# Kernel tuning notes

Hardware: AMD Instinct MI355X
Metric: run time of the kernel (lower is better)

The kernel has to match this reference:

```python
import jax, jax.numpy as jnp
import numpy as np

B, S, D, H = 2, 2048, 1024, 16
DK = D // H  # 64


def setup_inputs() -> dict:
    key = jax.random.key(0)
    ks = jax.random.split(key, 7)
    q = jax.random.normal(ks[0], (B, S, D), dtype=jnp.float32)
    k = jax.random.normal(ks[1], (B, S, D), dtype=jnp.float32)
    v = jax.random.normal(ks[2], (B, S, D), dtype=jnp.float32)
    # causal 0/1 mask, broadcast over batch and heads
    mask = jnp.tril(jnp.ones((S, S), dtype=jnp.int32))[None, None, :, :]
    scale = 0.02
    Wq = jax.random.normal(ks[3], (D, D), dtype=jnp.float32) * scale
    Wk = jax.random.normal(ks[4], (D, D), dtype=jnp.float32) * scale
    Wv = jax.random.normal(ks[5], (D, D), dtype=jnp.float32) * scale
    Wo = jax.random.normal(ks[6], (D, D), dtype=jnp.float32) * scale
    return {"q": q, "k": k, "v": v, "mask": mask,
            "Wq": Wq, "Wk": Wk, "Wv": Wv, "Wo": Wo}


def _split_heads(x):
    # [B, S, D] -> [B, H, S, DK]
    return x.reshape(B, -1, H, DK).transpose(0, 2, 1, 3)


def reference(q, k, v, mask, Wq, Wk, Wv, Wo):
    # torch nn.Linear(bias=False): y = x @ W.T
    qh = _split_heads(q @ Wq.T)
    kh = _split_heads(k @ Wk.T)
    vh = _split_heads(v @ Wv.T)
    scores = jnp.einsum('bhqd,bhkd->bhqk', qh, kh) / jnp.sqrt(
        jnp.asarray(DK, dtype=jnp.float32))
    scores = jnp.where(mask == 0, -jnp.inf, scores)
    attn = jax.nn.softmax(scores, axis=-1)              # [B, H, S, S]
    out = jnp.einsum('bhqk,bhkd->bhqd', attn, vh)        # [B, H, S, DK]
    concat = out.transpose(0, 2, 1, 3).reshape(B, -1, D)  # [B, S, D]
    return concat @ Wo.T, attn
```

## Files before the change

kernel.cpp:

```cpp
#include <hip/hip_runtime.h>
#include <hip/hip_bf16.h>
#include <stdint.h>

#define B_   2
#define S_   2048
#define D_   1024
#define H_   16
#define DK_  64

typedef __attribute__((ext_vector_type(4))) float          f32x4;
typedef __attribute__((ext_vector_type(8))) __bf16         bf16x8;
typedef __attribute__((ext_vector_type(8))) short          short8;
typedef __attribute__((ext_vector_type(4))) unsigned short u16x4;

__device__ __forceinline__ unsigned short f2bf(float x) {
  union { float f; unsigned u; } un; un.f = x;
  unsigned r = un.u + 0x7fffu + ((un.u >> 16) & 1u);
  return (unsigned short)(r >> 16);
}

__device__ __forceinline__ float fexp2(float x) {
  float r;
  asm("v_exp_f32 %0, %1" : "=v"(r) : "v"(x));
  return r;
}

#define WAIT_LGKM0() asm volatile("s_waitcnt lgkmcnt(0)" ::: "memory")
#define WAIT_VM0()   asm volatile("s_waitcnt vmcnt(0)" ::: "memory")
#define BAR()        __builtin_amdgcn_s_barrier()

#define ASYNC16(gp, lp)                                                         \
  __builtin_amdgcn_global_load_lds(                                             \
      (const __attribute__((address_space(1))) unsigned int*)(const void*)(gp), \
      (__attribute__((address_space(3))) unsigned int*)(void*)(lp), 16, 0, 0)

struct Cvt3 { const float* in[3]; unsigned short* out[3]; };
struct Cvt4 { const float* in[4]; unsigned short* out[4]; };

__global__ __launch_bounds__(256) void cvt3_kernel(Cvt3 a, int n4) {
  int z = blockIdx.y;
  int i = blockIdx.x * 256 + threadIdx.x;
  if (i >= n4) return;
  f32x4 v = *(const f32x4*)(a.in[z] + (size_t)i * 4);
  u16x4 o;
  o.x = f2bf(v.x); o.y = f2bf(v.y); o.z = f2bf(v.z); o.w = f2bf(v.w);
  *(u16x4*)(a.out[z] + (size_t)i * 4) = o;
}

__global__ __launch_bounds__(256) void cvt4_kernel(Cvt4 a, int n4) {
  int z = blockIdx.y;
  int i = blockIdx.x * 256 + threadIdx.x;
  if (i >= n4) return;
  f32x4 v = *(const f32x4*)(a.in[z] + (size_t)i * 4);
  u16x4 o;
  o.x = f2bf(v.x); o.y = f2bf(v.y); o.z = f2bf(v.z); o.w = f2bf(v.w);
  *(u16x4*)(a.out[z] + (size_t)i * 4) = o;
}

template <int BN>
__device__ __forceinline__ void gemm_core(const unsigned short* __restrict__ A,
                                          const unsigned short* __restrict__ W,
                                          unsigned short* sA, unsigned short* sB,
                                          int mBase, int nBase, f32x4 acc[4][BN / 32]) {
  constexpr int NW = BN / 32;
  const int tid = threadIdx.x, wid = tid >> 6, lane = tid & 63;
  const int g16 = lane >> 4, l16 = lane & 15;
  const int wr = wid >> 1, wc = wid & 1;

  auto stage = [&](int buf, int k0) {
#pragma unroll
    for (int i = 0; i < 2; ++i) {
      int L = i * 256 + tid;
      int row = L >> 2;
      int gsw = (L & 3) ^ (row & 3);
      ASYNC16(A + (size_t)(mBase + row) * 1024 + k0 + gsw * 8,
              sA + buf * (128 * 32) + (size_t)(i * 256 + wid * 64) * 8);
    }
#pragma unroll
    for (int i = 0; i < BN / 64; ++i) {
      int L = i * 256 + tid;
      int row = L >> 2;
      int gsw = (L & 3) ^ (row & 3);
      ASYNC16(W + (size_t)(nBase + row) * 1024 + k0 + gsw * 8,
              sB + buf * (BN * 32) + (size_t)(i * 256 + wid * 64) * 8);
    }
  };

  stage(0, 0);
  WAIT_VM0();
  BAR();
  for (int t = 0; t < 32; ++t) {
    const int cur = t & 1;
    if (t < 31) stage(cur ^ 1, (t + 1) * 32);
    const unsigned short* pA = sA + cur * (128 * 32);
    const unsigned short* pB = sB + cur * (BN * 32);
    bf16x8 a[4], b[NW];
#pragma unroll
    for (int mi = 0; mi < 4; ++mi) {
      int rr = wr * 64 + mi * 16 + l16;
      a[mi] = *(const bf16x8*)&pA[rr * 32 + ((g16 ^ (rr & 3)) * 8)];
    }
#pragma unroll
    for (int ni = 0; ni < NW; ++ni) {
      int rr = wc * (BN / 2) + ni * 16 + l16;
      b[ni] = *(const bf16x8*)&pB[rr * 32 + ((g16 ^ (rr & 3)) * 8)];
    }
#pragma unroll
    for (int mi = 0; mi < 4; ++mi)
#pragma unroll
      for (int ni = 0; ni < NW; ++ni)
        acc[mi][ni] = __builtin_amdgcn_mfma_f32_16x16x32_bf16(a[mi], b[ni],
                                                              acc[mi][ni], 0, 0, 0);
    WAIT_LGKM0();
    WAIT_VM0();
    BAR();
  }
}

struct QKVArgs {
  const unsigned short* A[3];
  const unsigned short* W[3];
  unsigned short* O[3];
};

__global__ __launch_bounds__(256) void gemm_qkv(QKVArgs args) {
  __shared__ unsigned short sA[2 * 128 * 32];
  __shared__ unsigned short sB[2 * 128 * 32];
  const int z = blockIdx.z;
  const int mBase = blockIdx.x * 128, nBase = blockIdx.y * 128;
  f32x4 acc[4][4];
  const f32x4 zz = {0.f, 0.f, 0.f, 0.f};
#pragma unroll
  for (int mi = 0; mi < 4; ++mi)
#pragma unroll
    for (int ni = 0; ni < 4; ++ni) acc[mi][ni] = zz;
  gemm_core<128>(args.A[z], args.W[z], sA, sB, mBase, nBase, acc);

  unsigned short* __restrict__ O = args.O[z];
  const int tid = threadIdx.x, wid = tid >> 6, lane = tid & 63;
  const int g16 = lane >> 4, l16 = lane & 15;
  const int wr = wid >> 1, wc = wid & 1;
  const float qscale = 0.125f * 1.44269504088896f;
  const float sc = (z == 0) ? qscale : 1.f;
#pragma unroll
  for (int mi = 0; mi < 4; ++mi)
#pragma unroll
    for (int ni = 0; ni < 4; ++ni)
#pragma unroll
      for (int r = 0; r < 4; ++r) {
        int row = mBase + wr * 64 + mi * 16 + g16 * 4 + r;
        int col = nBase + wc * 64 + ni * 16 + l16;
        int bb = row >> 11, ss = row & 2047;
        int hh = col >> 6,  dd = col & 63;
        unsigned short val = f2bf(acc[mi][ni][r] * sc);
        if (z == 2)
          O[((size_t)(bb * H_ + hh) * DK_ + dd) * S_ + ss] = val;
        else
          O[(((size_t)(bb * H_ + hh)) * S_ + ss) * DK_ + dd] = val;
      }
}

__global__ __launch_bounds__(256) void gemm_out(const unsigned short* __restrict__ A,
                                                const unsigned short* __restrict__ W,
                                                float* __restrict__ Cout) {
  __shared__ unsigned short sA[2 * 128 * 32];
  __shared__ unsigned short sB[2 * 64 * 32];
  const int mBase = blockIdx.x * 128, nBase = blockIdx.y * 64;
  f32x4 acc[4][2];
  const f32x4 zz = {0.f, 0.f, 0.f, 0.f};
#pragma unroll
  for (int mi = 0; mi < 4; ++mi)
#pragma unroll
    for (int ni = 0; ni < 2; ++ni) acc[mi][ni] = zz;
  gemm_core<64>(A, W, sA, sB, mBase, nBase, acc);

  const int tid = threadIdx.x, wid = tid >> 6, lane = tid & 63;
  const int g16 = lane >> 4, l16 = lane & 15;
  const int wr = wid >> 1, wc = wid & 1;
#pragma unroll
  for (int mi = 0; mi < 4; ++mi)
#pragma unroll
    for (int ni = 0; ni < 2; ++ni)
#pragma unroll
      for (int r = 0; r < 4; ++r) {
        int row = mBase + wr * 64 + mi * 16 + g16 * 4 + r;
        int col = nBase + wc * 32 + ni * 16 + l16;
        Cout[(size_t)row * 1024 + col] = acc[mi][ni][r];
      }
}

__global__ __launch_bounds__(256) void attn_kernel(
    const unsigned short* __restrict__ Qh, const unsigned short* __restrict__ Kh,
    const unsigned short* __restrict__ VhT, float* __restrict__ attn,
    unsigned short* __restrict__ Oc) {
  __shared__ unsigned short sK[2 * 64 * 64];
  __shared__ unsigned short sV[2 * 64 * 64];
  __shared__ unsigned short sP[64 * 64];
  const int tid = threadIdx.x, wid = tid >> 6, lane = tid & 63;
  const int g16 = lane >> 4, l16 = lane & 15;
  const int qb = (int)gridDim.x - 1 - (int)blockIdx.x;
  const int bh = blockIdx.y;
  const int qBase = qb * 64;
  const size_t headOff = (size_t)bh * S_ * DK_;
  const int jmax = qb;

  bf16x8 qf[2];
  {
    const unsigned short* qp = Qh + headOff + (size_t)(qBase + wid * 16 + l16) * DK_;
    qf[0] = *(const bf16x8*)(qp + g16 * 8);
    qf[1] = *(const bf16x8*)(qp + 32 + g16 * 8);
  }
  const int rowbase = qBase + wid * 16 + g16 * 4;

  auto stageK = [&](int buf, int j) {
#pragma unroll
    for (int i = 0; i < 2; ++i) {
      int L = i * 256 + tid;
      int krow = L >> 3;
      int gsw = (L & 7) ^ (krow & 7);
      ASYNC16(Kh + headOff + (size_t)(j * 64 + krow) * DK_ + gsw * 8,
              sK + buf * 4096 + (size_t)(i * 256 + wid * 64) * 8);
    }
  };
  auto stageV = [&](int buf, int j) {
#pragma unroll
    for (int i = 0; i < 2; ++i) {
      int L = i * 256 + tid;
      int vrow = L >> 3;
      int gsw = (L & 7) ^ (vrow & 7);
      ASYNC16(VhT + ((size_t)bh * DK_ + vrow) * S_ + j * 64 + gsw * 8,
              sV + buf * 4096 + (size_t)(i * 256 + wid * 64) * 8);
    }
  };

  float l4[4] = {0.f, 0.f, 0.f, 0.f};

  stageK(0, 0);
  WAIT_VM0();
  BAR();
  for (int j = 0; j <= jmax; ++j) {
    const int cur = j & 1;
    if (j < jmax) stageK(cur ^ 1, j + 1);
    const unsigned short* pK = sK + cur * 4096;
    f32x4 sc[4];
    const f32x4 zz = {0.f, 0.f, 0.f, 0.f};
#pragma unroll
    for (int ni = 0; ni < 4; ++ni) sc[ni] = zz;
#pragma unroll
    for (int ks = 0; ks < 2; ++ks)
#pragma unroll
      for (int ni = 0; ni < 4; ++ni) {
        int rr = ni * 16 + l16;
        bf16x8 kb = *(const bf16x8*)&pK[rr * 64 + (((ks * 4 + g16) ^ (rr & 7)) * 8)];
        sc[ni] = __builtin_amdgcn_mfma_f32_16x16x32_bf16(qf[ks], kb, sc[ni], 0, 0, 0);
      }
    if (j < jmax) {
#pragma unroll
      for (int ni = 0; ni < 4; ++ni)
#pragma unroll
        for (int r = 0; r < 4; ++r) l4[r] += fexp2(sc[ni][r]);
    } else {
#pragma unroll
      for (int ni = 0; ni < 4; ++ni) {
        int col = j * 64 + ni * 16 + l16;
#pragma unroll
        for (int r = 0; r < 4; ++r) {
          float e = fexp2(sc[ni][r]);
          l4[r] += (col <= rowbase + r) ? e : 0.f;
        }
      }
    }
    WAIT_LGKM0();
    WAIT_VM0();
    BAR();
  }

  float invl[4];
#pragma unroll
  for (int r = 0; r < 4; ++r) {
    float s = l4[r];
    s += __shfl_xor(s, 1);
    s += __shfl_xor(s, 2);
    s += __shfl_xor(s, 4);
    s += __shfl_xor(s, 8);
    invl[r] = 1.f / s;
  }

  f32x4 oacc[4];
  {
    const f32x4 zz = {0.f, 0.f, 0.f, 0.f};
#pragma unroll
    for (int ni = 0; ni < 4; ++ni) oacc[ni] = zz;
  }

  stageK(0, 0);
  stageV(0, 0);
  WAIT_VM0();
  BAR();
  for (int j = 0; j <= jmax; ++j) {
    const int cur = j & 1;
    if (j < jmax) { stageK(cur ^ 1, j + 1); stageV(cur ^ 1, j + 1); }
    const unsigned short* pK = sK + cur * 4096;
    const unsigned short* pV = sV + cur * 4096;
    f32x4 sc[4];
    const f32x4 zz = {0.f, 0.f, 0.f, 0.f};
#pragma unroll
    for (int ni = 0; ni < 4; ++ni) sc[ni] = zz;
#pragma unroll
    for (int ks = 0; ks < 2; ++ks)
#pragma unroll
      for (int ni = 0; ni < 4; ++ni) {
        int rr = ni * 16 + l16;
        bf16x8 kb = *(const bf16x8*)&pK[rr * 64 + (((ks * 4 + g16) ^ (rr & 7)) * 8)];
        sc[ni] = __builtin_amdgcn_mfma_f32_16x16x32_bf16(qf[ks], kb, sc[ni], 0, 0, 0);
      }
    float* arow = attn + ((size_t)bh * S_ + rowbase) * (size_t)S_ + j * 64;
    if (j < jmax) {
#pragma unroll
      for (int ni = 0; ni < 4; ++ni) {
        int cl = ni * 16 + l16;
#pragma unroll
        for (int r = 0; r < 4; ++r) {
          float p = fexp2(sc[ni][r]) * invl[r];
          arow[(size_t)r * S_ + cl] = p;
          int prow = wid * 16 + g16 * 4 + r;
          sP[prow * 64 + (((cl >> 3) ^ (prow & 7)) * 8) + (cl & 7)] = f2bf(p);
        }
      }
    } else {
#pragma unroll
      for (int ni = 0; ni < 4; ++ni) {
        int cl = ni * 16 + l16;
        int col = j * 64 + cl;
#pragma unroll
        for (int r = 0; r < 4; ++r) {
          float e = fexp2(sc[ni][r]) * invl[r];
          float p = (col <= rowbase + r) ? e : 0.f;
          arow[(size_t)r * S_ + cl] = p;
          int prow = wid * 16 + g16 * 4 + r;
          sP[prow * 64 + (((cl >> 3) ^ (prow & 7)) * 8) + (cl & 7)] = f2bf(p);
        }
      }
    }
#pragma unroll
    for (int ks = 0; ks < 2; ++ks) {
      int pr = wid * 16 + l16;
      bf16x8 pa = *(const bf16x8*)&sP[pr * 64 + (((ks * 4 + g16) ^ (pr & 7)) * 8)];
#pragma unroll
      for (int ni = 0; ni < 4; ++ni) {
        int vr = ni * 16 + l16;
        bf16x8 vb = *(const bf16x8*)&pV[vr * 64 + (((ks * 4 + g16) ^ (vr & 7)) * 8)];
        oacc[ni] = __builtin_amdgcn_mfma_f32_16x16x32_bf16(pa, vb, oacc[ni], 0, 0, 0);
      }
    }
    WAIT_LGKM0();
    WAIT_VM0();
    BAR();
  }

  const int bb = bh >> 4, hh = bh & 15;
#pragma unroll
  for (int ni = 0; ni < 4; ++ni)
#pragma unroll
    for (int r = 0; r < 4; ++r) {
      int srow = rowbase + r;
      Oc[((size_t)bb * S_ + srow) * D_ + hh * 64 + ni * 16 + l16] = f2bf(oacc[ni][r]);
    }

  const int zstart = (jmax + 1) * 64;
  if (zstart < S_) {
    const f32x4 z4 = {0.f, 0.f, 0.f, 0.f};
    int r = tid >> 2;
    int c0 = zstart + (tid & 3) * 4;
    float* rowp = attn + ((size_t)bh * S_ + qBase + r) * (size_t)S_;
    for (int c = c0; c < S_; c += 16)
      *(f32x4*)(rowp + c) = z4;
  }
}

extern "C" void kernel_launch(void* const* d_in, const int* in_sizes, int n_in,
                              void* d_out, int out_size, void* d_ws, size_t ws_size,
                              hipStream_t stream) {
  const float* q  = (const float*)d_in[0];
  const float* k  = (const float*)d_in[1];
  const float* v  = (const float*)d_in[2];
  const float* Wq = (const float*)d_in[4];
  const float* Wk = (const float*)d_in[5];
  const float* Wv = (const float*)d_in[6];
  const float* Wo = (const float*)d_in[7];

  float* out  = (float*)d_out;
  float* attn = out + (size_t)B_ * S_ * D_;

  unsigned short* ws = (unsigned short*)d_ws;
  const size_t BSD = (size_t)B_ * S_ * D_;
  const size_t DD  = (size_t)D_ * D_;
  unsigned short* qb  = ws;
  unsigned short* kb  = qb + BSD;
  unsigned short* vb  = kb + BSD;
  unsigned short* wqb = vb + BSD;
  unsigned short* wkb = wqb + DD;
  unsigned short* wvb = wkb + DD;
  unsigned short* wob = wvb + DD;
  unsigned short* Qh  = wob + DD;
  unsigned short* Kh  = Qh + BSD;
  unsigned short* VhT = Kh + BSD;
  unsigned short* Oc  = VhT + BSD;

  const int n4 = (int)(BSD / 4);
  const int w4 = (int)(DD / 4);
  Cvt3 c3; c3.in[0] = q; c3.in[1] = k; c3.in[2] = v;
  c3.out[0] = qb; c3.out[1] = kb; c3.out[2] = vb;
  cvt3_kernel<<<dim3(n4 / 256, 3), 256, 0, stream>>>(c3, n4);
  Cvt4 c4; c4.in[0] = Wq; c4.in[1] = Wk; c4.in[2] = Wv; c4.in[3] = Wo;
  c4.out[0] = wqb; c4.out[1] = wkb; c4.out[2] = wvb; c4.out[3] = wob;
  cvt4_kernel<<<dim3(w4 / 256, 4), 256, 0, stream>>>(c4, w4);

  QKVArgs args;
  args.A[0] = qb;  args.A[1] = kb;  args.A[2] = vb;
  args.W[0] = wqb; args.W[1] = wkb; args.W[2] = wvb;
  args.O[0] = Qh;  args.O[1] = Kh;  args.O[2] = VhT;
  gemm_qkv<<<dim3(32, 8, 3), 256, 0, stream>>>(args);

  attn_kernel<<<dim3(32, 32), 256, 0, stream>>>(Qh, Kh, VhT, attn, Oc);

  gemm_out<<<dim3(32, 16), 256, 0, stream>>>(Oc, wob, out);
}
```

Before: 282.7 us.

## Merge conversion kernels and swizzle GEMM block order across XCDs

Folds the two fp32-to-bf16 conversion launches into one seven-slice kernel. The projection GEMMs now use a flat grid whose block index is remapped so that consecutive blocks on each XCD (round-robin by 8) share A/W tiles, aiming for better L2 reuse. The manual waitcnt and barrier sequence is replaced with __syncthreads. The merged conversion launches many idle blocks for the smaller weight slices, and the remap assumes an 8-way XCD dispatch.

```diff
diff --git a/kernel.cpp b/kernel.cpp
--- a/kernel.cpp
+++ b/kernel.cpp
@@ -34,22 +34,12 @@
       (const __attribute__((address_space(1))) unsigned int*)(const void*)(gp), \
       (__attribute__((address_space(3))) unsigned int*)(void*)(lp), 16, 0, 0)
 
-struct Cvt3 { const float* in[3]; unsigned short* out[3]; };
-struct Cvt4 { const float* in[4]; unsigned short* out[4]; };
-
-__global__ __launch_bounds__(256) void cvt3_kernel(Cvt3 a, int n4) {
-  int z = blockIdx.y;
-  int i = blockIdx.x * 256 + threadIdx.x;
-  if (i >= n4) return;
-  f32x4 v = *(const f32x4*)(a.in[z] + (size_t)i * 4);
-  u16x4 o;
-  o.x = f2bf(v.x); o.y = f2bf(v.y); o.z = f2bf(v.z); o.w = f2bf(v.w);
-  *(u16x4*)(a.out[z] + (size_t)i * 4) = o;
-}
-
-__global__ __launch_bounds__(256) void cvt4_kernel(Cvt4 a, int n4) {
-  int z = blockIdx.y;
-  int i = blockIdx.x * 256 + threadIdx.x;
+struct CvtAll { const float* in[7]; unsigned short* out[7]; };
+
+__global__ __launch_bounds__(256) void cvt_all(CvtAll a, int n4big, int n4w) {
+  const int z = blockIdx.y;
+  const int n4 = (z < 3) ? n4big : n4w;
+  const int i = blockIdx.x * 256 + threadIdx.x;
   if (i >= n4) return;
   f32x4 v = *(const f32x4*)(a.in[z] + (size_t)i * 4);
   u16x4 o;
@@ -87,8 +77,7 @@
   };
 
   stage(0, 0);
-  WAIT_VM0();
-  BAR();
+  __syncthreads();
   for (int t = 0; t < 32; ++t) {
     const int cur = t & 1;
     if (t < 31) stage(cur ^ 1, (t + 1) * 32);
@@ -111,9 +100,7 @@
       for (int ni = 0; ni < NW; ++ni)
         acc[mi][ni] = __builtin_amdgcn_mfma_f32_16x16x32_bf16(a[mi], b[ni],
                                                               acc[mi][ni], 0, 0, 0);
-    WAIT_LGKM0();
-    WAIT_VM0();
-    BAR();
+    __syncthreads();
   }
 }
 
@@ -126,8 +113,12 @@
 __global__ __launch_bounds__(256) void gemm_qkv(QKVArgs args) {
   __shared__ unsigned short sA[2 * 128 * 32];
   __shared__ unsigned short sB[2 * 128 * 32];
-  const int z = blockIdx.z;
-  const int mBase = blockIdx.x * 128, nBase = blockIdx.y * 128;
+  const int flat = blockIdx.x;
+  const int swz = (flat & 7) * 96 + (flat >> 3);
+  const int z = swz >> 8;
+  const int rem = swz & 255;
+  const int mBase = (rem >> 3) * 128, nBase = (rem & 7) * 128;
+
   f32x4 acc[4][4];
   const f32x4 zz = {0.f, 0.f, 0.f, 0.f};
 #pragma unroll
@@ -165,7 +156,10 @@
                                                 float* __restrict__ Cout) {
   __shared__ unsigned short sA[2 * 128 * 32];
   __shared__ unsigned short sB[2 * 64 * 32];
-  const int mBase = blockIdx.x * 128, nBase = blockIdx.y * 64;
+  const int flat = blockIdx.x;
+  const int swz = (flat & 7) * 64 + (flat >> 3);
+  const int mBase = (swz >> 4) * 128, nBase = (swz & 15) * 64;
+
   f32x4 acc[4][2];
   const f32x4 zz = {0.f, 0.f, 0.f, 0.f};
 #pragma unroll
@@ -409,20 +403,20 @@
 
   const int n4 = (int)(BSD / 4);
   const int w4 = (int)(DD / 4);
-  Cvt3 c3; c3.in[0] = q; c3.in[1] = k; c3.in[2] = v;
-  c3.out[0] = qb; c3.out[1] = kb; c3.out[2] = vb;
-  cvt3_kernel<<<dim3(n4 / 256, 3), 256, 0, stream>>>(c3, n4);
-  Cvt4 c4; c4.in[0] = Wq; c4.in[1] = Wk; c4.in[2] = Wv; c4.in[3] = Wo;
-  c4.out[0] = wqb; c4.out[1] = wkb; c4.out[2] = wvb; c4.out[3] = wob;
-  cvt4_kernel<<<dim3(w4 / 256, 4), 256, 0, stream>>>(c4, w4);
+  CvtAll ca;
+  ca.in[0] = q;  ca.in[1] = k;  ca.in[2] = v;
+  ca.in[3] = Wq; ca.in[4] = Wk; ca.in[5] = Wv; ca.in[6] = Wo;
+  ca.out[0] = qb;  ca.out[1] = kb;  ca.out[2] = vb;
+  ca.out[3] = wqb; ca.out[4] = wkb; ca.out[5] = wvb; ca.out[6] = wob;
+  cvt_all<<<dim3(n4 / 256, 7), 256, 0, stream>>>(ca, n4, w4);
 
   QKVArgs args;
   args.A[0] = qb;  args.A[1] = kb;  args.A[2] = vb;
   args.W[0] = wqb; args.W[1] = wkb; args.W[2] = wvb;
   args.O[0] = Qh;  args.O[1] = Kh;  args.O[2] = VhT;
-  gemm_qkv<<<dim3(32, 8, 3), 256, 0, stream>>>(args);
+  gemm_qkv<<<dim3(768), 256, 0, stream>>>(args);
 
   attn_kernel<<<dim3(32, 32), 256, 0, stream>>>(Qh, Kh, VhT, attn, Oc);
 
-  gemm_out<<<dim3(32, 16), 256, 0, stream>>>(Oc, wob, out);
-}
+  gemm_out<<<dim3(512), 256, 0, stream>>>(Oc, wob, out);
+}
```

Measured after the change: 292.5 us. 3.4% more time.

## Process two 64-row query groups per attention block to reuse K/V tiles

Applied to the files above, without the earlier changes.

Each attention workgroup now handles 128 query rows as two 64-row groups that share every staged K and V tile, which halves the grid from 32x32 to 16x32 blocks. This cuts repeated global-to-LDS traffic for K/V and the per-block launch overhead. The cost is more registers for the doubled Q fragments and accumulators, fewer blocks to spread over the CUs, and some imbalance from the diagonal tile that only the second group computes. Zero-fill of the masked region is adjusted for the larger block.

```diff
diff --git a/kernel.cpp b/kernel.cpp
--- a/kernel.cpp
+++ b/kernel.cpp
@@ -200,17 +200,21 @@
   const int g16 = lane >> 4, l16 = lane & 15;
   const int qb = (int)gridDim.x - 1 - (int)blockIdx.x;
   const int bh = blockIdx.y;
-  const int qBase = qb * 64;
+  const int QBASE = qb * 128;
   const size_t headOff = (size_t)bh * S_ * DK_;
-  const int jmax = qb;
-
-  bf16x8 qf[2];
-  {
-    const unsigned short* qp = Qh + headOff + (size_t)(qBase + wid * 16 + l16) * DK_;
-    qf[0] = *(const bf16x8*)(qp + g16 * 8);
-    qf[1] = *(const bf16x8*)(qp + 32 + g16 * 8);
-  }
-  const int rowbase = qBase + wid * 16 + g16 * 4;
+  const int jmax = 2 * qb + 1;
+
+  bf16x8 qf[2][2];
+#pragma unroll
+  for (int g = 0; g < 2; ++g) {
+    const unsigned short* qp =
+        Qh + headOff + (size_t)(QBASE + g * 64 + wid * 16 + l16) * DK_;
+    qf[g][0] = *(const bf16x8*)(qp + g16 * 8);
+    qf[g][1] = *(const bf16x8*)(qp + 32 + g16 * 8);
+  }
+  int rowbase[2];
+  rowbase[0] = QBASE + wid * 16 + g16 * 4;
+  rowbase[1] = rowbase[0] + 64;
 
   auto stageK = [&](int buf, int j) {
 #pragma unroll
@@ -233,7 +237,7 @@
     }
   };
 
-  float l4[4] = {0.f, 0.f, 0.f, 0.f};
+  float l4[2][4] = {{0.f, 0.f, 0.f, 0.f}, {0.f, 0.f, 0.f, 0.f}};
 
   stageK(0, 0);
   WAIT_VM0();
@@ -242,31 +246,36 @@
     const int cur = j & 1;
     if (j < jmax) stageK(cur ^ 1, j + 1);
     const unsigned short* pK = sK + cur * 4096;
-    f32x4 sc[4];
-    const f32x4 zz = {0.f, 0.f, 0.f, 0.f};
-#pragma unroll
-    for (int ni = 0; ni < 4; ++ni) sc[ni] = zz;
-#pragma unroll
-    for (int ks = 0; ks < 2; ++ks)
-#pragma unroll
-      for (int ni = 0; ni < 4; ++ni) {
-        int rr = ni * 16 + l16;
-        bf16x8 kb = *(const bf16x8*)&pK[rr * 64 + (((ks * 4 + g16) ^ (rr & 7)) * 8)];
-        sc[ni] = __builtin_amdgcn_mfma_f32_16x16x32_bf16(qf[ks], kb, sc[ni], 0, 0, 0);
-      }
-    if (j < jmax) {
-#pragma unroll
-      for (int ni = 0; ni < 4; ++ni)
-#pragma unroll
-        for (int r = 0; r < 4; ++r) l4[r] += fexp2(sc[ni][r]);
-    } else {
-#pragma unroll
-      for (int ni = 0; ni < 4; ++ni) {
-        int col = j * 64 + ni * 16 + l16;
-#pragma unroll
-        for (int r = 0; r < 4; ++r) {
-          float e = fexp2(sc[ni][r]);
-          l4[r] += (col <= rowbase + r) ? e : 0.f;
+#pragma unroll
+    for (int g = 0; g < 2; ++g) {
+      const int dg = 2 * qb + g;
+      if (j > dg) continue;
+      f32x4 sc[4];
+      const f32x4 zz = {0.f, 0.f, 0.f, 0.f};
+#pragma unroll
+      for (int ni = 0; ni < 4; ++ni) sc[ni] = zz;
+#pragma unroll
+      for (int ks = 0; ks < 2; ++ks)
+#pragma unroll
+        for (int ni = 0; ni < 4; ++ni) {
+          int rr = ni * 16 + l16;
+          bf16x8 kb = *(const bf16x8*)&pK[rr * 64 + (((ks * 4 + g16) ^ (rr & 7)) * 8)];
+          sc[ni] = __builtin_amdgcn_mfma_f32_16x16x32_bf16(qf[g][ks], kb, sc[ni], 0, 0, 0);
+        }
+      if (j < dg) {
+#pragma unroll
+        for (int ni = 0; ni < 4; ++ni)
+#pragma unroll
+          for (int r = 0; r < 4; ++r) l4[g][r] += fexp2(sc[ni][r]);
+      } else {
+#pragma unroll
+        for (int ni = 0; ni < 4; ++ni) {
+          int col = j * 64 + ni * 16 + l16;
+#pragma unroll
+          for (int r = 0; r < 4; ++r) {
+            float e = fexp2(sc[ni][r]);
+            l4[g][r] += (col <= rowbase[g] + r) ? e : 0.f;
+          }
         }
       }
     }
@@ -275,22 +284,26 @@
     BAR();
   }
 
-  float invl[4];
-#pragma unroll
-  for (int r = 0; r < 4; ++r) {
-    float s = l4[r];
-    s += __shfl_xor(s, 1);
-    s += __shfl_xor(s, 2);
-    s += __shfl_xor(s, 4);
-    s += __shfl_xor(s, 8);
-    invl[r] = 1.f / s;
-  }
-
-  f32x4 oacc[4];
+  float invl[2][4];
+#pragma unroll
+  for (int g = 0; g < 2; ++g)
+#pragma unroll
+    for (int r = 0; r < 4; ++r) {
+      float s = l4[g][r];
+      s += __shfl_xor(s, 1);
+      s += __shfl_xor(s, 2);
+      s += __shfl_xor(s, 4);
+      s += __shfl_xor(s, 8);
+      invl[g][r] = 1.f / s;
+    }
+
+  f32x4 oacc[2][4];
   {
     const f32x4 zz = {0.f, 0.f, 0.f, 0.f};
 #pragma unroll
-    for (int ni = 0; ni < 4; ++ni) oacc[ni] = zz;
+    for (int g = 0; g < 2; ++g)
+#pragma unroll
+      for (int ni = 0; ni < 4; ++ni) oacc[g][ni] = zz;
   }
 
   stageK(0, 0);
@@ -302,55 +315,69 @@
     if (j < jmax) { stageK(cur ^ 1, j + 1); stageV(cur ^ 1, j + 1); }
     const unsigned short* pK = sK + cur * 4096;
     const unsigned short* pV = sV + cur * 4096;
-    f32x4 sc[4];
-    const f32x4 zz = {0.f, 0.f, 0.f, 0.f};
-#pragma unroll
-    for (int ni = 0; ni < 4; ++ni) sc[ni] = zz;
-#pragma unroll
-    for (int ks = 0; ks < 2; ++ks)
-#pragma unroll
-      for (int ni = 0; ni < 4; ++ni) {
-        int rr = ni * 16 + l16;
-        bf16x8 kb = *(const bf16x8*)&pK[rr * 64 + (((ks * 4 + g16) ^ (rr & 7)) * 8)];
-        sc[ni] = __builtin_amdgcn_mfma_f32_16x16x32_bf16(qf[ks], kb, sc[ni], 0, 0, 0);
-      }
-    float* arow = attn + ((size_t)bh * S_ + rowbase) * (size_t)S_ + j * 64;
-    if (j < jmax) {
-#pragma unroll
-      for (int ni = 0; ni < 4; ++ni) {
-        int cl = ni * 16 + l16;
-#pragma unroll
-        for (int r = 0; r < 4; ++r) {
-          float p = fexp2(sc[ni][r]) * invl[r];
-          arow[(size_t)r * S_ + cl] = p;
-          int prow = wid * 16 + g16 * 4 + r;
-          sP[prow * 64 + (((cl >> 3) ^ (prow & 7)) * 8) + (cl & 7)] = f2bf(p);
-        }
-      }
-    } else {
-#pragma unroll
-      for (int ni = 0; ni < 4; ++ni) {
-        int cl = ni * 16 + l16;
-        int col = j * 64 + cl;
-#pragma unroll
-        for (int r = 0; r < 4; ++r) {
-          float e = fexp2(sc[ni][r]) * invl[r];
-          float p = (col <= rowbase + r) ? e : 0.f;
-          arow[(size_t)r * S_ + cl] = p;
-          int prow = wid * 16 + g16 * 4 + r;
-          sP[prow * 64 + (((cl >> 3) ^ (prow & 7)) * 8) + (cl & 7)] = f2bf(p);
-        }
-      }
-    }
-#pragma unroll
-    for (int ks = 0; ks < 2; ++ks) {
-      int pr = wid * 16 + l16;
-      bf16x8 pa = *(const bf16x8*)&sP[pr * 64 + (((ks * 4 + g16) ^ (pr & 7)) * 8)];
-#pragma unroll
-      for (int ni = 0; ni < 4; ++ni) {
-        int vr = ni * 16 + l16;
-        bf16x8 vb = *(const bf16x8*)&pV[vr * 64 + (((ks * 4 + g16) ^ (vr & 7)) * 8)];
-        oacc[ni] = __builtin_amdgcn_mfma_f32_16x16x32_bf16(pa, vb, oacc[ni], 0, 0, 0);
+#pragma unroll
+    for (int g = 0; g < 2; ++g) {
+      const int dg = 2 * qb + g;
+      float* arow = attn + ((size_t)bh * S_ + rowbase[g]) * (size_t)S_ + j * 64;
+      if (j > dg) {
+#pragma unroll
+        for (int ni = 0; ni < 4; ++ni) {
+          int cl = ni * 16 + l16;
+#pragma unroll
+          for (int r = 0; r < 4; ++r)
+            arow[(size_t)r * S_ + cl] = 0.f;
+        }
+        continue;
+      }
+      f32x4 sc[4];
+      const f32x4 zz = {0.f, 0.f, 0.f, 0.f};
+#pragma unroll
+      for (int ni = 0; ni < 4; ++ni) sc[ni] = zz;
+#pragma unroll
+      for (int ks = 0; ks < 2; ++ks)
+#pragma unroll
+        for (int ni = 0; ni < 4; ++ni) {
+          int rr = ni * 16 + l16;
+          bf16x8 kb = *(const bf16x8*)&pK[rr * 64 + (((ks * 4 + g16) ^ (rr & 7)) * 8)];
+          sc[ni] = __builtin_amdgcn_mfma_f32_16x16x32_bf16(qf[g][ks], kb, sc[ni], 0, 0, 0);
+        }
+      if (j < dg) {
+#pragma unroll
+        for (int ni = 0; ni < 4; ++ni) {
+          int cl = ni * 16 + l16;
+#pragma unroll
+          for (int r = 0; r < 4; ++r) {
+            float p = fexp2(sc[ni][r]) * invl[g][r];
+            arow[(size_t)r * S_ + cl] = p;
+            int prow = wid * 16 + g16 * 4 + r;
+            sP[prow * 64 + (((cl >> 3) ^ (prow & 7)) * 8) + (cl & 7)] = f2bf(p);
+          }
+        }
+      } else {
+#pragma unroll
+        for (int ni = 0; ni < 4; ++ni) {
+          int cl = ni * 16 + l16;
+          int col = j * 64 + cl;
+#pragma unroll
+          for (int r = 0; r < 4; ++r) {
+            float e = fexp2(sc[ni][r]) * invl[g][r];
+            float p = (col <= rowbase[g] + r) ? e : 0.f;
+            arow[(size_t)r * S_ + cl] = p;
+            int prow = wid * 16 + g16 * 4 + r;
+            sP[prow * 64 + (((cl >> 3) ^ (prow & 7)) * 8) + (cl & 7)] = f2bf(p);
+          }
+        }
+      }
+#pragma unroll
+      for (int ks = 0; ks < 2; ++ks) {
+        int pr = wid * 16 + l16;
+        bf16x8 pa = *(const bf16x8*)&sP[pr * 64 + (((ks * 4 + g16) ^ (pr & 7)) * 8)];
+#pragma unroll
+        for (int ni = 0; ni < 4; ++ni) {
+          int vr = ni * 16 + l16;
+          bf16x8 vb = *(const bf16x8*)&pV[vr * 64 + (((ks * 4 + g16) ^ (vr & 7)) * 8)];
+          oacc[g][ni] = __builtin_amdgcn_mfma_f32_16x16x32_bf16(pa, vb, oacc[g][ni], 0, 0, 0);
+        }
       }
     }
     WAIT_LGKM0();
@@ -360,20 +387,22 @@
 
   const int bb = bh >> 4, hh = bh & 15;
 #pragma unroll
-  for (int ni = 0; ni < 4; ++ni)
-#pragma unroll
-    for (int r = 0; r < 4; ++r) {
-      int srow = rowbase + r;
-      Oc[((size_t)bb * S_ + srow) * D_ + hh * 64 + ni * 16 + l16] = f2bf(oacc[ni][r]);
-    }
+  for (int g = 0; g < 2; ++g)
+#pragma unroll
+    for (int ni = 0; ni < 4; ++ni)
+#pragma unroll
+      for (int r = 0; r < 4; ++r) {
+        int srow = rowbase[g] + r;
+        Oc[((size_t)bb * S_ + srow) * D_ + hh * 64 + ni * 16 + l16] = f2bf(oacc[g][ni][r]);
+      }
 
   const int zstart = (jmax + 1) * 64;
   if (zstart < S_) {
     const f32x4 z4 = {0.f, 0.f, 0.f, 0.f};
-    int r = tid >> 2;
-    int c0 = zstart + (tid & 3) * 4;
-    float* rowp = attn + ((size_t)bh * S_ + qBase + r) * (size_t)S_;
-    for (int c = c0; c < S_; c += 16)
+    int r = tid >> 1;
+    int c0 = zstart + (tid & 1) * 4;
+    float* rowp = attn + ((size_t)bh * S_ + QBASE + r) * (size_t)S_;
+    for (int c = c0; c < S_; c += 8)
       *(f32x4*)(rowp + c) = z4;
   }
 }
@@ -422,7 +451,7 @@
   args.O[0] = Qh;  args.O[1] = Kh;  args.O[2] = VhT;
   gemm_qkv<<<dim3(32, 8, 3), 256, 0, stream>>>(args);
 
-  attn_kernel<<<dim3(32, 32), 256, 0, stream>>>(Qh, Kh, VhT, attn, Oc);
+  attn_kernel<<<dim3(16, 32), 256, 0, stream>>>(Qh, Kh, VhT, attn, Oc);
 
   gemm_out<<<dim3(32, 16), 256, 0, stream>>>(Oc, wob, out);
 }
```

New measurement: 291.3 us. +3.0%, slower.
